# Performance work log

Hardware: AMD Instinct MI355X
Metric: run time of the kernel (lower is better)

## Reference

```python
import jax, jax.numpy as jnp
import numpy as np

K = 3
STRIDE = 1
PADDING = 1


def _conv2d(x, w, b, stride, padding):
    out = jax.lax.conv_general_dilated(
        x, w, window_strides=(stride, stride),
        padding=[(padding, padding), (padding, padding)],
        dimension_numbers=('NCHW', 'OIHW', 'NCHW'))
    return out + b[None, :, None, None]


def _grid_sample_bilinear_zeros(x, grid):
    B, C, Hin, Win = x.shape
    gx = (grid[..., 0] + 1.0) * (Win * 0.5) - 0.5  # (B,Hg,Wg) pixel coords
    gy = (grid[..., 1] + 1.0) * (Hin * 0.5) - 0.5
    x0f = jnp.floor(gx)
    y0f = jnp.floor(gy)
    wx1 = gx - x0f  # bilinear weights
    wy1 = gy - y0f
    x0 = x0f.astype(jnp.int32)
    y0 = y0f.astype(jnp.int32)
    xf = x.reshape(B, C, Hin * Win)

    def gather(yi, xi):
        valid = (xi >= 0) & (xi < Win) & (yi >= 0) & (yi < Hin)  # zero padding
        idx = jnp.clip(yi, 0, Hin - 1) * Win + jnp.clip(xi, 0, Win - 1)
        g = jax.vmap(lambda xb, ib: xb[:, ib])(xf, idx)  # (B,C,Hg,Wg)
        return g * valid[:, None, :, :].astype(x.dtype)

    w00 = ((1.0 - wx1) * (1.0 - wy1))[:, None]
    w01 = (wx1 * (1.0 - wy1))[:, None]
    w10 = ((1.0 - wx1) * wy1)[:, None]
    w11 = (wx1 * wy1)[:, None]
    return (gather(y0, x0) * w00 + gather(y0, x0 + 1) * w01 +
            gather(y0 + 1, x0) * w10 + gather(y0 + 1, x0 + 1) * w11)


def setup_inputs() -> dict:
    key = jax.random.key(0)
    k1, k2, k3 = jax.random.split(key, 3)
    B, C, O, H, W = 8, 128, 128, 64, 64
    x = jax.random.normal(k1, (B, C, H, W), dtype=jnp.float32)
    # small offset-predictor weights so sampled locations stay near the grid
    w_off = jax.random.normal(k2, (2 * K * K, C, K, K), dtype=jnp.float32) * 1e-3
    b_off = jnp.zeros((2 * K * K,), dtype=jnp.float32)
    w_main = jax.random.normal(k3, (O, C, K, K), dtype=jnp.float32) * 0.05
    b_main = jnp.zeros((O,), dtype=jnp.float32)
    return {"x": x, "w_off": w_off, "b_off": b_off, "w_main": w_main, "b_main": b_main}


def reference(x, w_off, b_off, w_main, b_main):
    offset = _conv2d(x, w_off, b_off, STRIDE, PADDING)  # (B, 2*K*K, H, W)
    B, _, H, W = offset.shape
    off = jnp.transpose(offset, (0, 2, 3, 1)).reshape(B, H, W, K, K, 2)
    # The torch in-place loops reduce to:
    #   x-comp: cumsum over i of column j=0, broadcast over j
    #   y-comp: cumsum over j of row    i=0, broadcast over i
    ox = jnp.cumsum(off[:, :, :, :, 0, 0], axis=3)  # (B,H,W,K)
    oy = jnp.cumsum(off[:, :, :, 0, :, 1], axis=3)  # (B,H,W,K)
    ox_f = jnp.broadcast_to(ox[..., None], (B, H, W, K, K))
    oy_f = jnp.broadcast_to(oy[:, :, :, None, :], (B, H, W, K, K))
    off_f = jnp.stack([ox_f, oy_f], axis=-1).reshape(B, H, W, K * K, 2)

    y_range = jnp.linspace(-1.0, 1.0, H, dtype=x.dtype)
    x_range = jnp.linspace(-1.0, 1.0, W, dtype=x.dtype)
    yg, xg = jnp.meshgrid(y_range, x_range, indexing='ij')
    base = jnp.stack((xg, yg), axis=-1)  # (H,W,2)
    grid = base[None, :, :, None, :] + off_f  # (B,H,W,K*K,2)
    grid = grid.reshape(B, H, W * K * K, 2)

    xs = _grid_sample_bilinear_zeros(x, grid)  # (B,C,H,W*K*K)
    C = x.shape[1]
    xs = xs.reshape(B, C, H, W, K * K)
    wm = w_main.reshape(w_main.shape[0], C, K * K)
    out = jnp.einsum('bchwk,ock->bohw', xs, wm)
    return out + b_main[None, :, None, None]
```

## Files before the change

### kernel.cpp

```cpp
#include <hip/hip_runtime.h>
#include <hip/hip_bf16.h>
#include <stdint.h>

typedef unsigned short u16;
typedef unsigned int u32;
typedef __attribute__((ext_vector_type(8))) short short8;
typedef __attribute__((ext_vector_type(4))) float float4v;

#define CH 128
#define OO 128
#define KD 1152
#define MPIX 32768

__device__ __forceinline__ u16 f2bf(float v) {
    __hip_bfloat16 h = __float2bfloat16(v);
    return *reinterpret_cast<u16*>(&h);
}

__device__ __forceinline__ float bf_lo(u32 u) {
    u32 t = u << 16;
    return __builtin_bit_cast(float, t);
}
__device__ __forceinline__ float bf_hi(u32 u) {
    u32 t = u & 0xffff0000u;
    return __builtin_bit_cast(float, t);
}
__device__ __forceinline__ u32 pack_bf16(float lo, float hi) {
    u32 ul = __builtin_bit_cast(u32, lo);
    u32 uh = __builtin_bit_cast(u32, hi);
    return ((ul + 0x8000u) >> 16) | ((uh + 0x8000u) & 0xffff0000u);
}

__global__ __launch_bounds__(256) void transpose_kernel(const float* __restrict__ x,
                                                        __hip_bfloat16* __restrict__ xt) {
    __shared__ float st[64][65];
    int tid = threadIdx.x;
    int bh = blockIdx.x;
    int b = bh >> 6;
    int h = bh & 63;
    const float* xb = x + ((size_t)b * CH) * 4096 + (size_t)h * 64;
    __hip_bfloat16* xo = xt + ((size_t)bh << 6) * CH;
    for (int cc0 = 0; cc0 < 128; cc0 += 64) {
        #pragma unroll
        for (int step = 0; step < 16; ++step) {
            int cl = (tid >> 6) + step * 4;
            int w = tid & 63;
            st[cl][w] = xb[(size_t)(cc0 + cl) * 4096 + w];
        }
        __syncthreads();
        #pragma unroll
        for (int step = 0; step < 16; ++step) {
            int w = (tid >> 6) + step * 4;
            int cl = tid & 63;
            xo[(size_t)w * CH + cc0 + cl] = __float2bfloat16(st[cl][w]);
        }
        __syncthreads();
    }
}

__global__ __launch_bounds__(256) void offset_conv_kernel(const float* __restrict__ x,
                                                          const float* __restrict__ w_off,
                                                          float* __restrict__ partial) {
    int tid = threadIdx.x;
    int m = blockIdx.x * 256 + tid;
    int chunk = blockIdx.y;
    int b = m >> 12;
    int hw = m & 4095;
    int h = hw >> 6;
    int w = hw & 63;
    float acc[6] = {0.f, 0.f, 0.f, 0.f, 0.f, 0.f};
    int c0 = chunk * 32;
    for (int c = c0; c < c0 + 32; ++c) {
        const float* xc = x + ((size_t)(b * CH + c) << 12);
        float xv[9];
        #pragma unroll
        for (int dy = 0; dy < 3; ++dy) {
            int yy = h + dy - 1;
            bool vy = (unsigned)yy < 64u;
            #pragma unroll
            for (int dx = 0; dx < 3; ++dx) {
                int xx = w + dx - 1;
                bool vv = vy && ((unsigned)xx < 64u);
                xv[dy * 3 + dx] = vv ? xc[yy * 64 + xx] : 0.f;
            }
        }
        const float* wb = w_off + (size_t)c * 9;
        #pragma unroll
        for (int s = 0; s < 6; ++s) {
            int chn = (s < 3) ? s * 6 : (s - 3) * 2 + 1;
            const float* wp = wb + (size_t)chn * (CH * 9);
            float a = acc[s];
            #pragma unroll
            for (int t = 0; t < 9; ++t) a = fmaf(xv[t], wp[t], a);
            acc[s] = a;
        }
    }
    float* po = partial + ((size_t)(chunk << 15) + m) * 6;
    #pragma unroll
    for (int s = 0; s < 6; ++s) po[s] = acc[s];
}

__global__ __launch_bounds__(256) void wreorder_kernel(const float* __restrict__ w_main,
                                                       u16* __restrict__ Wb) {
    int idx = blockIdx.x * 256 + threadIdx.x;
    if (idx >= OO * KD) return;
    int o = idx / KD;
    int r = idx - o * KD;
    int k = r >> 7;
    int c = r & 127;
    Wb[idx] = f2bf(w_main[(size_t)o * KD + c * 9 + k]);
}

__global__ __launch_bounds__(256) void fused_gemm_kernel(const __hip_bfloat16* __restrict__ xt,
                                                         const float* __restrict__ partial,
                                                         const float* __restrict__ b_off,
                                                         const u16* __restrict__ Wb,
                                                         const float* __restrict__ b_main,
                                                         float* __restrict__ out) {
    __shared__ float offs[64][6];
    __shared__ __align__(16) float4v twt[64][9];
    __shared__ __align__(16) int4 tbs[64][9];
    __shared__ __align__(16) u16 lA[128 * 32];
    __shared__ __align__(16) u16 lB[64 * 32];

    int tid = threadIdx.x;
    int m0 = blockIdx.x * 64;
    int b = m0 >> 12;
    int h = (m0 & 4095) >> 6;

    for (int idx = tid; idx < 64 * 6; idx += 256) {
        int pix = idx / 6, s = idx % 6;
        int m = m0 + pix;
        int chn = (s < 3) ? s * 6 : (s - 3) * 2 + 1;
        float v = b_off[chn];
        #pragma unroll
        for (int q = 0; q < 4; ++q) v += partial[((size_t)(q << 15) + m) * 6 + s];
        offs[pix][s] = v;
    }
    __syncthreads();

    for (int idx = tid; idx < 64 * 9; idx += 256) {
        int pix = idx / 9, k = idx % 9;
        int i = k / 3, j = k - i * 3;
        float ox = offs[pix][0];
        if (i >= 1) ox += offs[pix][1];
        if (i >= 2) ox += offs[pix][2];
        float oy = offs[pix][3];
        if (j >= 1) oy += offs[pix][4];
        if (j >= 2) oy += offs[pix][5];
        const float step = 2.0f / 63.0f;
        float bxn = -1.0f + pix * step;
        float byn = -1.0f + h * step;
        float gx = fmaf(bxn + ox, 32.0f, 31.5f);
        float gy = fmaf(byn + oy, 32.0f, 31.5f);
        float x0f = floorf(gx), y0f = floorf(gy);
        float wx = gx - x0f, wy = gy - y0f;
        int ix0 = (int)x0f, iy0 = (int)y0f;
        int ix1 = ix0 + 1, iy1 = iy0 + 1;
        float fx0 = ((unsigned)ix0 < 64u) ? 1.f : 0.f;
        float fx1 = ((unsigned)ix1 < 64u) ? 1.f : 0.f;
        float fy0 = ((unsigned)iy0 < 64u) ? 1.f : 0.f;
        float fy1 = ((unsigned)iy1 < 64u) ? 1.f : 0.f;
        float4v wv;
        wv[0] = (1.f - wy) * (1.f - wx) * fy0 * fx0;
        wv[1] = (1.f - wy) * wx * fy0 * fx1;
        wv[2] = wy * (1.f - wx) * fy1 * fx0;
        wv[3] = wy * wx * fy1 * fx1;
        int cx0 = min(max(ix0, 0), 63), cx1 = min(max(ix1, 0), 63);
        int cy0 = min(max(iy0, 0), 63), cy1 = min(max(iy1, 0), 63);
        twt[pix][k] = wv;
        tbs[pix][k] = make_int4((cy0 * 64 + cx0) * 64, (cy0 * 64 + cx1) * 64,
                                (cy1 * 64 + cx0) * 64, (cy1 * 64 + cx1) * 64);
    }
    __syncthreads();

    int wave = tid >> 6, lane = tid & 63;
    int wo = wave & 1;
    int wp = wave >> 1;
    int mrow = lane & 15;
    int q8 = (lane >> 4) * 8;

    int pix = tid >> 2;
    int cg = (tid & 3) * 8;
    const u32* xb = (const u32*)(xt + (((size_t)b << 12) * (size_t)CH));
    const u16* abase = Wb + (size_t)(tid >> 2) * KD + (tid & 3) * 8;
    int asto = (tid >> 2) * 32 + (tid & 3) * 8;
    int bsto = pix * 32 + cg;

    float4v acc[4][2];
    #pragma unroll
    for (int sm = 0; sm < 4; ++sm)
        #pragma unroll
        for (int sn = 0; sn < 2; ++sn)
            acc[sm][sn] = (float4v){0.f, 0.f, 0.f, 0.f};

    float4v wv;
    int4 bv;
    uint4 u00, u01, u10, u11, a0, a1;

    auto issue = [&](int kk) {
        if ((kk & 3) == 0) {
            int k = kk >> 2;
            wv = twt[pix][k];
            bv = tbs[pix][k];
        }
        const u32* xc = xb + ((((kk & 3) << 5) + cg) >> 1);
        u00 = *(const uint4*)(xc + bv.x);
        u01 = *(const uint4*)(xc + bv.y);
        u10 = *(const uint4*)(xc + bv.z);
        u11 = *(const uint4*)(xc + bv.w);
        const u16* ap = abase + kk * 32;
        a0 = *(const uint4*)ap;
        a1 = *(const uint4*)(ap + (size_t)64 * KD);
    };

    issue(0);

    for (int kk = 0; kk < 36; ++kk) {
        *(uint4*)&lA[asto] = a0;
        *(uint4*)&lA[asto + 64 * 32] = a1;
        {
            const u32* p00 = (const u32*)&u00;
            const u32* p01 = (const u32*)&u01;
            const u32* p10 = (const u32*)&u10;
            const u32* p11 = (const u32*)&u11;
            u32 outp[4];
            #pragma unroll
            for (int q = 0; q < 4; ++q) {
                float lo = wv[0] * bf_lo(p00[q]);
                lo = fmaf(wv[1], bf_lo(p01[q]), lo);
                lo = fmaf(wv[2], bf_lo(p10[q]), lo);
                lo = fmaf(wv[3], bf_lo(p11[q]), lo);
                float hi = wv[0] * bf_hi(p00[q]);
                hi = fmaf(wv[1], bf_hi(p01[q]), hi);
                hi = fmaf(wv[2], bf_hi(p10[q]), hi);
                hi = fmaf(wv[3], bf_hi(p11[q]), hi);
                outp[q] = pack_bf16(lo, hi);
            }
            *(uint4*)&lB[bsto] = *(const uint4*)outp;
        }
        __syncthreads();

        if (kk < 35) issue(kk + 1);

        short8 af[4], bfv[2];
        #pragma unroll
        for (int s = 0; s < 4; ++s)
            af[s] = *(const short8*)&lA[(wo * 64 + s * 16 + mrow) * 32 + q8];
        #pragma unroll
        for (int s = 0; s < 2; ++s)
            bfv[s] = *(const short8*)&lB[(wp * 32 + s * 16 + mrow) * 32 + q8];
        #pragma unroll
        for (int sm = 0; sm < 4; ++sm)
            #pragma unroll
            for (int sn = 0; sn < 2; ++sn)
                acc[sm][sn] = __builtin_amdgcn_mfma_f32_16x16x32_bf16(af[sm], bfv[sn],
                                                                     acc[sm][sn], 0, 0, 0);
        __syncthreads();
    }

    #pragma unroll
    for (int sm = 0; sm < 4; ++sm) {
        int o = wo * 64 + sm * 16 + (lane >> 4) * 4;
        #pragma unroll
        for (int sn = 0; sn < 2; ++sn) {
            int pcol = m0 + wp * 32 + sn * 16 + mrow;
            int rem = pcol & 4095;
            float* op = out + (((size_t)b * OO) << 12) + rem;
            #pragma unroll
            for (int r = 0; r < 4; ++r)
                op[(size_t)(o + r) << 12] = acc[sm][sn][r] + b_main[o + r];
        }
    }
}

extern "C" void kernel_launch(void* const* d_in, const int* in_sizes, int n_in,
                              void* d_out, int out_size, void* d_ws, size_t ws_size,
                              hipStream_t stream) {
    const float* x      = (const float*)d_in[0];
    const float* w_off  = (const float*)d_in[1];
    const float* b_off  = (const float*)d_in[2];
    const float* w_main = (const float*)d_in[3];
    const float* b_main = (const float*)d_in[4];
    float* out = (float*)d_out;

    char* ws = (char*)d_ws;
    __hip_bfloat16* xt = (__hip_bfloat16*)ws;
    float* partial = (float*)(ws + 8388608);
    u16* Wb   = (u16*)(ws + 8388608 + 3145728);

    transpose_kernel<<<512, 256, 0, stream>>>(x, xt);
    offset_conv_kernel<<<dim3(128, 4), 256, 0, stream>>>(x, w_off, partial);
    wreorder_kernel<<<576, 256, 0, stream>>>(w_main, Wb);
    fused_gemm_kernel<<<MPIX / 64, 256, 0, stream>>>(xt, partial, b_off, Wb, b_main, out);
}
```

Before: 137.1 us.

## Double-buffer LDS tiles, drop trailing barrier, remap blocks, pack bilinear math

Makes the A and B shared-memory tiles double-buffered so each k-step needs only one barrier instead of two. The next step's global loads are issued before that barrier. The block index is remapped so consecutive blocks walk across batches rather than rows, which changes L2 locality for the gathers. The bilinear interpolation is rewritten with two-float vectors so it can compile to packed FMAs. The cost is double the LDS footprint for the tiles, which may reduce occupancy, and the reordered issue extends register live ranges.

```diff
diff --git a/kernel.cpp b/kernel.cpp
--- a/kernel.cpp
+++ b/kernel.cpp
@@ -6,6 +6,7 @@
 typedef unsigned int u32;
 typedef __attribute__((ext_vector_type(8))) short short8;
 typedef __attribute__((ext_vector_type(4))) float float4v;
+typedef __attribute__((ext_vector_type(2))) float float2v;
 
 #define CH 128
 #define OO 128
@@ -24,6 +25,12 @@
 __device__ __forceinline__ float bf_hi(u32 u) {
     u32 t = u & 0xffff0000u;
     return __builtin_bit_cast(float, t);
+}
+__device__ __forceinline__ float2v unpk(u32 u) {
+    float2v r;
+    r.x = bf_lo(u);
+    r.y = bf_hi(u);
+    return r;
 }
 __device__ __forceinline__ u32 pack_bf16(float lo, float hi) {
     u32 ul = __builtin_bit_cast(u32, lo);
@@ -120,13 +127,14 @@
     __shared__ float offs[64][6];
     __shared__ __align__(16) float4v twt[64][9];
     __shared__ __align__(16) int4 tbs[64][9];
-    __shared__ __align__(16) u16 lA[128 * 32];
-    __shared__ __align__(16) u16 lB[64 * 32];
+    __shared__ __align__(16) u16 lA[2][128 * 32];
+    __shared__ __align__(16) u16 lB[2][64 * 32];
 
     int tid = threadIdx.x;
-    int m0 = blockIdx.x * 64;
-    int b = m0 >> 12;
-    int h = (m0 & 4095) >> 6;
+    int orig = blockIdx.x;
+    int b = orig & 7;
+    int h = orig >> 3;
+    int m0 = ((b << 6) + h) << 6;
 
     for (int idx = tid; idx < 64 * 6; idx += 256) {
         int pix = idx / 6, s = idx % 6;
@@ -217,8 +225,12 @@
     issue(0);
 
     for (int kk = 0; kk < 36; ++kk) {
-        *(uint4*)&lA[asto] = a0;
-        *(uint4*)&lA[asto + 64 * 32] = a1;
+        int cur = kk & 1;
+        u16* lAc = &lA[cur][0];
+        u16* lBc = &lB[cur][0];
+
+        *(uint4*)&lAc[asto] = a0;
+        *(uint4*)&lAc[asto + 64 * 32] = a1;
         {
             const u32* p00 = (const u32*)&u00;
             const u32* p01 = (const u32*)&u01;
@@ -227,36 +239,32 @@
             u32 outp[4];
             #pragma unroll
             for (int q = 0; q < 4; ++q) {
-                float lo = wv[0] * bf_lo(p00[q]);
-                lo = fmaf(wv[1], bf_lo(p01[q]), lo);
-                lo = fmaf(wv[2], bf_lo(p10[q]), lo);
-                lo = fmaf(wv[3], bf_lo(p11[q]), lo);
-                float hi = wv[0] * bf_hi(p00[q]);
-                hi = fmaf(wv[1], bf_hi(p01[q]), hi);
-                hi = fmaf(wv[2], bf_hi(p10[q]), hi);
-                hi = fmaf(wv[3], bf_hi(p11[q]), hi);
-                outp[q] = pack_bf16(lo, hi);
+                float2v p = unpk(p00[q]) * wv[0];
+                p += unpk(p01[q]) * wv[1];
+                p += unpk(p10[q]) * wv[2];
+                p += unpk(p11[q]) * wv[3];
+                outp[q] = pack_bf16(p.x, p.y);
             }
-            *(uint4*)&lB[bsto] = *(const uint4*)outp;
-        }
+            *(uint4*)&lBc[bsto] = *(const uint4*)outp;
+        }
+
+        if (kk < 35) issue(kk + 1);
+
         __syncthreads();
 
-        if (kk < 35) issue(kk + 1);
-
         short8 af[4], bfv[2];
         #pragma unroll
         for (int s = 0; s < 4; ++s)
-            af[s] = *(const short8*)&lA[(wo * 64 + s * 16 + mrow) * 32 + q8];
+            af[s] = *(const short8*)&lAc[(wo * 64 + s * 16 + mrow) * 32 + q8];
         #pragma unroll
         for (int s = 0; s < 2; ++s)
-            bfv[s] = *(const short8*)&lB[(wp * 32 + s * 16 + mrow) * 32 + q8];
+            bfv[s] = *(const short8*)&lBc[(wp * 32 + s * 16 + mrow) * 32 + q8];
         #pragma unroll
         for (int sm = 0; sm < 4; ++sm)
             #pragma unroll
             for (int sn = 0; sn < 2; ++sn)
                 acc[sm][sn] = __builtin_amdgcn_mfma_f32_16x16x32_bf16(af[sm], bfv[sn],
                                                                      acc[sm][sn], 0, 0, 0);
-        __syncthreads();
     }
 
     #pragma unroll
```

Measured after the change: 134.8 us. No clear change (-1.7%).
